# Kernel optimization log

Measured on AMD Instinct MI355X. Metric: run time of the kernel, lower is better.

Reference implementation:

```python
import jax, jax.numpy as jnp
import numpy as np

MAX_LEVEL = 3
FULL_LEN = 2 ** MAX_LEVEL  # wavelet_full_len for db1, mode='zero'


def _make_patterns():
    # Per-feature input to the DWT is [v, 0, ..., 0] (scalar zero-padded to 2**j).
    # Haar/db1 'zero' DWT of that signal is v times a fixed sparse pattern:
    # cA (len 1) = v*2^(-j/2); cD_k first element = v*2^(-k/2), rest zeros.
    pats = []
    for j in range(1, MAX_LEVEL + 1):
        vec = [2.0 ** (-j / 2.0)]                      # cA, length 1
        for k in range(1, j + 1):                      # cD_1 .. cD_j
            seg = np.zeros(2 ** (j - k))
            seg[0] = 2.0 ** (-k / 2.0)
            vec.extend(seg.tolist())
        full = np.zeros(FULL_LEN, dtype=np.float32)
        arr = np.asarray(vec, dtype=np.float32)
        full[: arr.shape[0]] = arr                     # F.pad to wavelet_full_len
        pats.append(full)
    return jnp.asarray(np.stack(pats))                 # (MAX_LEVEL, FULL_LEN)

_P = _make_patterns()


def _gumbel_hard(logits, gumb):
    # F.gumbel_softmax(logits, tau=1.0, hard=True), one sample per feature row.
    y = jax.nn.softmax(logits[None, :] + gumb, axis=-1)          # (feat, L)
    hard = jax.nn.one_hot(jnp.argmax(y, axis=-1), y.shape[-1], dtype=y.dtype)
    return jax.lax.stop_gradient(hard - y) + y                   # straight-through


def _wavelet_layer(x, logits, gumb, Wnl, bnl, Wwo, bwo):
    # Collapses the per-feature/per-level torch double loop:
    # xi_wave(level j) = v * (Wnl[f] . P[j]) + bnl[f]
    a = Wnl @ _P.T                       # (feat, levels)
    w = _gumbel_hard(logits, gumb)       # (feat, levels), one-hot rows
    coeff = jnp.sum(w * a, axis=-1)      # (feat,)
    agg = x * coeff + bnl                # (B, N, feat)
    return agg @ Wwo + bwo               # linear_out


def _mix(h, res_proj):
    diff = jnp.mean((h - res_proj) ** 2)
    th = jax.nn.sigmoid(diff)
    return th * h + (1.0 - th) * res_proj


def reference(x, adj, Wres, bres,
              Wg0, bg0, Wrg0, brg0, logits0, gumb0, Wnl0, bnl0, Wwo0, bwo0, Wrw0, brw0,
              Wg1, bg1, Wrg1, brg1, logits1, gumb1, Wnl1, bnl1, Wwo1, bwo1, Wrw1, brw1):
    res = x @ Wres + bres                                        # (B,N,Dout)
    # ---- layer 0 ----
    xg = jnp.einsum('ij,bjf->bif', adj, x) @ Wg0 + bg0           # 64->256: no residual add
    xg = _mix(xg, res @ Wrg0 + brg0)
    xw = _wavelet_layer(xg, logits0, gumb0, Wnl0, bnl0, Wwo0, bwo0) + xg  # 256==256: add
    xw = _mix(xw, res @ Wrw0 + brw0)
    # ---- layer 1 ----
    xg1 = jnp.einsum('ij,bjf->bif', adj, xw) @ Wg1 + bg1 + xw    # 256==256: add
    xg1 = _mix(xg1, res @ Wrg1 + brg1)
    xw1 = _wavelet_layer(xg1, logits1, gumb1, Wnl1, bnl1, Wwo1, bwo1)     # 256->64: no add
    xw1 = _mix(xw1, res @ Wrw1 + brw1)
    return xw1


def setup_inputs() -> dict:
    key = jax.random.key(0)
    ks = jax.random.split(key, 32)
    B, N, D_in, H, D_out = 128, 512, 64, 256, 64
    s = 0.05
    inp = {
        'x': jax.random.normal(ks[0], (B, N, D_in), jnp.float32),
        'adj': jax.random.uniform(ks[1], (N, N), jnp.float32) / N,
        'Wres': jax.random.normal(ks[2], (D_in, D_out), jnp.float32) * s,
        'bres': jax.random.normal(ks[3], (D_out,), jnp.float32) * s,
        'Wg0': jax.random.normal(ks[4], (D_in, H), jnp.float32) * s,
        'bg0': jax.random.normal(ks[5], (H,), jnp.float32) * s,
        'Wrg0': jax.random.normal(ks[6], (D_out, H), jnp.float32) * s,
        'brg0': jax.random.normal(ks[7], (H,), jnp.float32) * s,
        'logits0': jax.random.normal(ks[8], (3,), jnp.float32),
        'gumb0': jax.random.gumbel(ks[9], (H, 3), jnp.float32),
        'Wnl0': jax.random.normal(ks[10], (H, FULL_LEN), jnp.float32) * s,
        'bnl0': jax.random.normal(ks[11], (H,), jnp.float32) * s,
        'Wwo0': jax.random.normal(ks[12], (H, H), jnp.float32) * s,
        'bwo0': jax.random.normal(ks[13], (H,), jnp.float32) * s,
        'Wrw0': jax.random.normal(ks[14], (D_out, H), jnp.float32) * s,
        'brw0': jax.random.normal(ks[15], (H,), jnp.float32) * s,
        'Wg1': jax.random.normal(ks[16], (H, H), jnp.float32) * s,
        'bg1': jax.random.normal(ks[17], (H,), jnp.float32) * s,
        'Wrg1': jax.random.normal(ks[18], (D_out, H), jnp.float32) * s,
        'brg1': jax.random.normal(ks[19], (H,), jnp.float32) * s,
        'logits1': jax.random.normal(ks[20], (3,), jnp.float32),
        'gumb1': jax.random.gumbel(ks[21], (H, 3), jnp.float32),
        'Wnl1': jax.random.normal(ks[22], (H, FULL_LEN), jnp.float32) * s,
        'bnl1': jax.random.normal(ks[23], (H,), jnp.float32) * s,
        'Wwo1': jax.random.normal(ks[24], (H, D_out), jnp.float32) * s,
        'bwo1': jax.random.normal(ks[25], (D_out,), jnp.float32) * s,
        'Wrw1': jax.random.normal(ks[26], (D_out, D_out), jnp.float32) * s,
        'brw1': jax.random.normal(ks[27], (D_out,), jnp.float32) * s,
    }
    return inp
```

## Files before the change

### kernel.cpp

```cpp
#include <hip/hip_runtime.h>
#include <hip/hip_bf16.h>
#include <math.h>

#define BB   128
#define NN   512
#define DIN  64
#define HH   256
#define DOUT 64
#define BNR  (BB * NN)

typedef float  f32x4  __attribute__((ext_vector_type(4)));
typedef __bf16 bf16x8 __attribute__((ext_vector_type(8)));

#define GLP(p)  ((const __attribute__((address_space(1))) void*)(p))
#define LDSP(p) ((__attribute__((address_space(3))) void*)(p))

__constant__ float PAT[3][8] = {
    {0.70710678f, 0.70710678f, 0.f, 0.f, 0.f, 0.f, 0.f, 0.f},
    {0.5f,        0.70710678f, 0.f, 0.5f, 0.f, 0.f, 0.f, 0.f},
    {0.35355339f, 0.70710678f, 0.f, 0.f, 0.f, 0.5f, 0.f, 0.35355339f}
};

__device__ __forceinline__ unsigned short f2bfu(float x) {
    __hip_bfloat16 b = __float2bfloat16(x);
    unsigned short u;
    __builtin_memcpy(&u, &b, 2);
    return u;
}
__device__ __forceinline__ float bf2f(unsigned short u) {
    unsigned int v = ((unsigned int)u) << 16;
    float f;
    __builtin_memcpy(&f, &v, 4);
    return f;
}

__device__ __forceinline__ float block_th(const float* __restrict__ partial, int np,
                                          float inv_n, float* red, int tid)
{
    float s = 0.f;
    for (int i = tid; i < np; i += 256) s += partial[i];
    red[tid] = s;
    __syncthreads();
    for (int o = 128; o > 0; o >>= 1) {
        if (tid < o) red[tid] += red[tid + o];
        __syncthreads();
    }
    float th = 1.f / (1.f + expf(-red[0] * inv_n));
    __syncthreads();
    return th;
}

template<int BM, int BN, int FM, int FN>
__device__ __forceinline__ void write_tile(char* lds, f32x4 (&a)[FM][FN],
                                           __hip_bfloat16* __restrict__ C,
                                           long base, int N, int tid)
{
    const int wave = tid >> 6;
    const int lane = tid & 63;
    const int wm = wave >> 1, wn = wave & 1;
    const int lc = lane & 15;
    const int lr4 = (lane >> 4) << 2;
    __syncthreads();
    #pragma unroll
    for (int j = 0; j < FN; ++j) {
        int colb = (wn * (FN * 16) + j * 16 + lc) * 2;
        #pragma unroll
        for (int i = 0; i < FM; ++i) {
            int row0 = wm * (FM * 16) + i * 16 + lr4;
            #pragma unroll
            for (int r = 0; r < 4; ++r) {
                int row = row0 + r;
                *reinterpret_cast<unsigned short*>(
                    lds + row * (BN * 2) + (colb ^ (((row >> 2) & 3) << 5))) =
                    f2bfu(a[i][j][r]);
            }
        }
    }
    __syncthreads();
    const int TPR = BN / 8;
    const int RPP = 256 / TPR;
    #pragma unroll
    for (int p = 0; p < BM / RPP; ++p) {
        int row = p * RPP + tid / TPR;
        int cb = (tid % TPR) * 16;
        int pb = cb ^ (((row >> 2) & 3) << 5);
        uint4 v = *reinterpret_cast<const uint4*>(lds + row * (BN * 2) + pb);
        *reinterpret_cast<uint4*>(reinterpret_cast<char*>(C + base + (long)row * N) + cb) = v;
    }
}

template<int BM, int BN>
__device__ __forceinline__ void stage_tiles(const __hip_bfloat16* __restrict__ Ab,
                                            const __hip_bfloat16* __restrict__ Bb,
                                            char* AsB, char* BsB,
                                            int m0, int n0, int k0, int KA, int KB,
                                            int wave, int lane)
{
    const int NCH = (BM + BN) / 32;
    const int lr = lane >> 3;
    const int ls = lane & 7;
    #pragma unroll
    for (int cc = 0; cc < NCH; ++cc) {
        int c = wave * NCH + cc;
        const __hip_bfloat16* src;
        char* ldsb;
        if (c < BM / 8) {
            int r = c * 8 + lr;
            ldsb = AsB + c * 1024;
            src = Ab + ((long)(m0 + r) * KA + k0 + ((ls ^ (r & 7)) << 3));
        } else {
            int c2 = c - BM / 8;
            int r = c2 * 8 + lr;
            ldsb = BsB + c2 * 1024;
            src = Bb + ((long)(n0 + r) * KB + k0 + ((ls ^ (r & 7)) << 3));
        }
        __builtin_amdgcn_global_load_lds(GLP(src), LDSP(ldsb), 16, 0, 0);
    }
}

template<int BM, int BN, int FM, int FN>
__device__ __forceinline__ void mfma_tiles(char* AsB, char* BsB,
                                           f32x4 (&acc)[FM][FN], int wave, int lane)
{
    const int wm = wave >> 1, wn = wave & 1;
    #pragma unroll
    for (int ksl = 0; ksl < 2; ++ksl) {
        bf16x8 af[FM], bfr[FN];
        #pragma unroll
        for (int i = 0; i < FM; ++i) {
            int row = wm * (FM * 16) + i * 16 + (lane & 15);
            int off = (ksl * 64 + ((lane >> 4) << 4)) ^ ((row & 7) << 4);
            af[i] = *reinterpret_cast<const bf16x8*>(AsB + row * 128 + off);
        }
        #pragma unroll
        for (int j = 0; j < FN; ++j) {
            int row = wn * (FN * 16) + j * 16 + (lane & 15);
            int off = (ksl * 64 + ((lane >> 4) << 4)) ^ ((row & 7) << 4);
            bfr[j] = *reinterpret_cast<const bf16x8*>(BsB + row * 128 + off);
        }
        #pragma unroll
        for (int i = 0; i < FM; ++i)
            #pragma unroll
            for (int j = 0; j < FN; ++j)
                acc[i][j] = __builtin_amdgcn_mfma_f32_16x16x32_bf16(
                    af[i], bfr[j], acc[i][j], 0, 0, 0);
    }
}

__global__ __launch_bounds__(256) void cvt_k(const float* __restrict__ in,
                                             unsigned short* __restrict__ out, long n4)
{
    long gid = (long)blockIdx.x * 256 + threadIdx.x;
    long stride = (long)gridDim.x * 256;
    for (long i = gid; i < n4; i += stride) {
        float4 v = reinterpret_cast<const float4*>(in)[i];
        ushort4 u;
        u.x = f2bfu(v.x); u.y = f2bfu(v.y); u.z = f2bfu(v.z); u.w = f2bfu(v.w);
        reinterpret_cast<ushort4*>(out)[i] = u;
    }
}

__global__ __launch_bounds__(256) void cvtx_k(const float* __restrict__ in,
                                              unsigned short* __restrict__ rm,
                                              unsigned short* __restrict__ tr)
{
    __shared__ float t[64][65];
    const long base = (long)blockIdx.z * NN * DIN;
    const int r0 = blockIdx.y * 64;
    const int tr4 = threadIdx.x >> 6;
    const int tc  = threadIdx.x & 63;
    #pragma unroll
    for (int i = 0; i < 16; ++i) {
        int r = i * 4 + tr4;
        float v = in[base + (long)(r0 + r) * DIN + tc];
        t[r][tc] = v;
        rm[base + (long)(r0 + r) * DIN + tc] = f2bfu(v);
    }
    __syncthreads();
    #pragma unroll
    for (int i = 0; i < 16; ++i) {
        int d = i * 4 + tr4;
        tr[base + (long)d * NN + r0 + tc] = f2bfu(t[tc][d]);
    }
}

__device__ __forceinline__ void tcvt_body(const float* __restrict__ in,
                                          unsigned short* __restrict__ out,
                                          const float* __restrict__ cs, float us,
                                          int R, int C, int r0, int c0)
{
    __shared__ float t[64][65];
    int tr = threadIdx.x >> 6;
    int tc = threadIdx.x & 63;
    #pragma unroll
    for (int i = 0; i < 16; ++i) {
        int r = i * 4 + tr;
        t[r][tc] = in[(long)(r0 + r) * C + c0 + tc];
    }
    __syncthreads();
    float sc = (cs ? cs[r0 + tc] : 1.0f) * us;
    #pragma unroll
    for (int i = 0; i < 16; ++i) {
        int r = i * 4 + tr;
        out[(long)(c0 + r) * R + r0 + tc] = f2bfu(t[tc][r] * sc);
    }
}

struct WTArgs {
    const float* src[8];
    unsigned short* dst[8];
    const float* cs[8];
    float sgn[8];
    int R[8], C[8];
};
__global__ __launch_bounds__(256) void tcvt_w_k(WTArgs a)
{
    int wgt = blockIdx.y;
    int R = a.R[wgt], C = a.C[wgt];
    int tilesX = C >> 6;
    int tiles = (R >> 6) * tilesX;
    int t = blockIdx.x;
    if (t >= tiles) return;
    tcvt_body(a.src[wgt], a.dst[wgt], a.cs[wgt], a.sgn[wgt], R, C,
              (t / tilesX) * 64, (t % tilesX) * 64);
}

__global__ void coeff_k(const float* __restrict__ logits, const float* __restrict__ gumb,
                        const float* __restrict__ Wnl, float* __restrict__ coeff)
{
    int f = threadIdx.x;
    float l0 = logits[0] + gumb[f * 3 + 0];
    float l1 = logits[1] + gumb[f * 3 + 1];
    float l2 = logits[2] + gumb[f * 3 + 2];
    int bl = 0;
    float bv = l0;
    if (l1 > bv) { bv = l1; bl = 1; }
    if (l2 > bv) { bv = l2; bl = 2; }
    float s = 0.f;
    #pragma unroll
    for (int t = 0; t < 8; ++t) s += Wnl[f * 8 + t] * PAT[bl][t];
    coeff[f] = s;
}

struct FVArgs {
    const float* W[5];
    const float* c[5];
    const float* v[5];
    const float* base[5];
    float* out[5];
    int K[5], N[5];
};
__global__ __launch_bounds__(256) void foldvec_k(FVArgs a)
{
    int cs = blockIdx.y;
    int n = blockIdx.x;
    if (n >= a.N[cs]) return;
    int k = threadIdx.x;
    float s = 0.f;
    if (k < a.K[cs]) {
        float cc = a.c[cs] ? a.c[cs][k] : 1.0f;
        s = a.v[cs][k] * cc * a.W[cs][(long)k * a.N[cs] + n];
    }
    __shared__ float sm[256];
    sm[threadIdx.x] = s;
    __syncthreads();
    for (int o = 128; o > 0; o >>= 1) {
        if (threadIdx.x < o) sm[threadIdx.x] += sm[threadIdx.x + o];
        __syncthreads();
    }
    if (threadIdx.x == 0)
        a.out[cs][n] = (a.base[cs] ? a.base[cs][n] : 0.f) + sm[0];
}

struct WFArgs {
    const float* Wsrc[3];
    const float* Wbig[3];
    const float* c[3];
    int incl[3], N[3];
    unsigned short* dst[3];
};
__global__ __launch_bounds__(256) void wfold_k(WFArgs a)
{
    int cs = blockIdx.y;
    int m = blockIdx.x;
    __shared__ float ws[256];
    ws[threadIdx.x] = a.Wsrc[cs][m * 256 + threadIdx.x] * a.c[cs][threadIdx.x];
    __syncthreads();
    int n = threadIdx.x;
    int N = a.N[cs];
    if (n >= N) return;
    float s = a.incl[cs] ? a.Wsrc[cs][m * 256 + n] : 0.f;
    const float* Wb = a.Wbig[cs];
    #pragma unroll 8
    for (int k = 0; k < 256; ++k)
        s += ws[k] * Wb[(long)k * N + n];
    a.dst[cs][n * 64 + m] = f2bfu(s);
}

__global__ __launch_bounds__(256) void sc0_k(
    const float* __restrict__ partial, int np, float inv_n,
    unsigned short* __restrict__ Wa,
    unsigned short* __restrict__ Wb,
    const float* __restrict__ bg0p, const float* __restrict__ brg0p,
    const float* __restrict__ crow0, float* __restrict__ cv0)
{
    __shared__ float red[256];
    float th = block_th(partial, np, inv_n, red, threadIdx.x);
    float om = 1.f - th;
    int g = blockIdx.x * 256 + threadIdx.x;
    Wa[g] = f2bfu(th * bf2f(Wa[g]));
    Wb[g] = f2bfu(om * bf2f(Wb[g]));
    if (g < 256) cv0[g] = th * bg0p[g] + om * brg0p[g] + crow0[g];
}

__global__ __launch_bounds__(256) void sc1_k(
    const float* __restrict__ partial, int np, float inv_n,
    const unsigned short* __restrict__ Wrw0T, unsigned short* __restrict__ Wrw0sT,
    unsigned short* __restrict__ Wg0pT, unsigned short* __restrict__ Wrg0pT,
    const float* __restrict__ bg1, const float* __restrict__ brw0,
    const float* __restrict__ cv0, float* __restrict__ bv1g)
{
    __shared__ float red[256];
    float th = block_th(partial, np, inv_n, red, threadIdx.x);
    float om = 1.f - th;
    int g = blockIdx.x * 256 + threadIdx.x;
    Wrw0sT[g] = f2bfu(om * bf2f(Wrw0T[g]));
    Wg0pT[g]  = f2bfu(th * bf2f(Wg0pT[g]));
    Wrg0pT[g] = f2bfu(th * bf2f(Wrg0pT[g]));
    if (g < 256) bv1g[g] = bg1[g] + om * brw0[g] + th * cv0[g];
}

__global__ __launch_bounds__(256) void sc2_k(
    const float* __restrict__ partial, int np, float inv_n,
    unsigned short* __restrict__ Wc1T,
    unsigned short* __restrict__ Wrgc1T,
    const float* __restrict__ brgc1, const float* __restrict__ crow1,
    float* __restrict__ cv2)
{
    __shared__ float red[256];
    float th = block_th(partial, np, inv_n, red, threadIdx.x);
    float om = 1.f - th;
    int g = blockIdx.x * 256 + threadIdx.x;
    Wc1T[g] = f2bfu(th * bf2f(Wc1T[g]));
    if (g < 4096) Wrgc1T[g] = f2bfu(om * bf2f(Wrgc1T[g]));
    if (g < 64) cv2[g] = om * brgc1[g] + crow1[g];
}

template<int BM, int BN, int FM, int FN>
__global__ __launch_bounds__(256) void gemm_bt_k(
    const __hip_bfloat16* __restrict__ A, const __hip_bfloat16* __restrict__ Bt,
    const float* __restrict__ bias, __hip_bfloat16* __restrict__ Cb,
    int M, int N, int K)
{
    __shared__ __attribute__((aligned(128))) char lds[(BM + BN) * 128];
    char* AsB = lds;
    char* BsB = lds + BM * 128;

    const int m0 = blockIdx.y * BM;
    const int n0 = blockIdx.x * BN;
    const int tid  = threadIdx.x;
    const int wave = tid >> 6;
    const int lane = tid & 63;
    const int wn = wave & 1;

    f32x4 acc[FM][FN];
    #pragma unroll
    for (int i = 0; i < FM; ++i)
        #pragma unroll
        for (int j = 0; j < FN; ++j)
            acc[i][j] = (f32x4){0.f, 0.f, 0.f, 0.f};

    for (int k0 = 0; k0 < K; k0 += 64) {
        stage_tiles<BM, BN>(A, Bt, AsB, BsB, m0, n0, k0, K, K, wave, lane);
        __syncthreads();
        mfma_tiles<BM, BN, FM, FN>(AsB, BsB, acc, wave, lane);
        __syncthreads();
    }

    const int lc = lane & 15;
    #pragma unroll
    for (int j = 0; j < FN; ++j) {
        int col = n0 + wn * (FN * 16) + j * 16 + lc;
        float bv = bias ? bias[col] : 0.0f;
        #pragma unroll
        for (int i = 0; i < FM; ++i)
            #pragma unroll
            for (int r = 0; r < 4; ++r)
                acc[i][j][r] += bv;
    }
    write_tile<BM, BN, FM, FN>(lds, acc, Cb, (long)m0 * N + n0, N, tid);
}

template<int BM, int BN, int FM, int FN, int GX, int NB>
__global__ __launch_bounds__(256) void gemm_bt_swz_k(
    const __hip_bfloat16* __restrict__ A, const __hip_bfloat16* __restrict__ Bt,
    __hip_bfloat16* __restrict__ Cb,
    int M, int N, int K, long sA, long sB, long sC)
{
    __shared__ __attribute__((aligned(128))) char lds[(BM + BN) * 128];
    char* AsB = lds;
    char* BsB = lds + BM * 128;

    const int d   = blockIdx.x;
    const int xcd = d & 7;
    const int q   = d >> 3;
    const int t   = q % NB;
    const int bz  = xcd + ((q / NB) << 3);
    const int n0  = (t % GX) * BN;
    const int m0  = (t / GX) * BM;

    const __hip_bfloat16* Ab = A + (long)bz * sA;
    const __hip_bfloat16* Bb = Bt + (long)bz * sB;

    const int tid  = threadIdx.x;
    const int wave = tid >> 6;
    const int lane = tid & 63;
    const int wn = wave & 1;

    f32x4 acc[FM][FN];
    #pragma unroll
    for (int i = 0; i < FM; ++i)
        #pragma unroll
        for (int j = 0; j < FN; ++j)
            acc[i][j] = (f32x4){0.f, 0.f, 0.f, 0.f};

    for (int k0 = 0; k0 < K; k0 += 64) {
        stage_tiles<BM, BN>(Ab, Bb, AsB, BsB, m0, n0, k0, K, K, wave, lane);
        __syncthreads();
        mfma_tiles<BM, BN, FM, FN>(AsB, BsB, acc, wave, lane);
        __syncthreads();
    }

    write_tile<BM, BN, FM, FN>(lds, acc, Cb, (long)bz * sC + (long)m0 * N + n0, N, tid);
}

template<int BM, int BN, int FM, int FN>
__global__ __launch_bounds__(256) void dual1_k(
    const __hip_bfloat16* __restrict__ A0, const __hip_bfloat16* __restrict__ B0, int K0,
    const __hip_bfloat16* __restrict__ A1, const __hip_bfloat16* __restrict__ B1, int K1,
    const float* __restrict__ b1, const float* __restrict__ b2,
    float* __restrict__ partial, int M, int N)
{
    __shared__ __attribute__((aligned(128))) char lds[(BM + BN) * 128];
    char* AsB = lds;
    char* BsB = lds + BM * 128;

    const int d   = blockIdx.x;
    const int q   = d >> 3;
    const int nx  = q & 1;
    const int my  = (d & 7) + ((q >> 1) << 3);
    const int m0  = my * BM;
    const int n0  = nx * BN;

    const int tid  = threadIdx.x;
    const int wave = tid >> 6;
    const int lane = tid & 63;
    const int wn = wave & 1;

    f32x4 acc[FM][FN];
    #pragma unroll
    for (int i = 0; i < FM; ++i)
        #pragma unroll
        for (int j = 0; j < FN; ++j)
            acc[i][j] = (f32x4){0.f, 0.f, 0.f, 0.f};

    #pragma unroll
    for (int ph = 0; ph < 2; ++ph) {
        const __hip_bfloat16* Ab = ph ? A1 : A0;
        const __hip_bfloat16* Bb = ph ? B1 : B0;
        const int K = ph ? K1 : K0;
        for (int k0 = 0; k0 < K; k0 += 64) {
            stage_tiles<BM, BN>(Ab, Bb, AsB, BsB, m0, n0, k0, K, K, wave, lane);
            __syncthreads();
            mfma_tiles<BM, BN, FM, FN>(AsB, BsB, acc, wave, lane);
            __syncthreads();
        }
    }

    const int lc = lane & 15;
    float dsum = 0.f;
    #pragma unroll
    for (int j = 0; j < FN; ++j) {
        int col = n0 + wn * (FN * 16) + j * 16 + lc;
        float bd = b1[col] - b2[col];
        #pragma unroll
        for (int i = 0; i < FM; ++i)
            #pragma unroll
            for (int r = 0; r < 4; ++r) {
                float dd = acc[i][j][r] + bd;
                dsum += dd * dd;
            }
    }

    float* red = (float*)lds;
    red[tid] = dsum;
    __syncthreads();
    for (int o = 128; o > 0; o >>= 1) {
        if (tid < o) red[tid] += red[tid + o];
        __syncthreads();
    }
    if (tid == 0) partial[my * 2 + nx] = red[0];
}

template<int BM, int BN, int FM, int FN, bool SWZ>
__global__ __launch_bounds__(256) void wave2_k(
    const __hip_bfloat16* __restrict__ A0, const __hip_bfloat16* __restrict__ B0, int K0,
    const __hip_bfloat16* __restrict__ A1, const __hip_bfloat16* __restrict__ B1, int K1,
    const __hip_bfloat16* __restrict__ A2, const __hip_bfloat16* __restrict__ B2, int K2,
    const float* __restrict__ cv, const float* __restrict__ b2v,
    __hip_bfloat16* __restrict__ C1, __hip_bfloat16* __restrict__ C2,
    float* __restrict__ partial_out, int M, int N)
{
    __shared__ __attribute__((aligned(128))) char lds[(BM + BN) * 128];
    char* AsB = lds;
    char* BsB = lds + BM * 128;

    int m0, n0, pidx;
    if constexpr (SWZ) {
        const int d = blockIdx.x;
        const int q = d >> 3;
        const int nx = q & 1;
        const int my = (d & 7) + ((q >> 1) << 3);
        m0 = my * BM; n0 = nx * BN; pidx = my * 2 + nx;
    } else {
        m0 = blockIdx.y * BM; n0 = blockIdx.x * BN;
        pidx = blockIdx.y * gridDim.x + blockIdx.x;
    }

    const int tid  = threadIdx.x;
    const int wave = tid >> 6;
    const int lane = tid & 63;
    const int wn = wave & 1;

    f32x4 acc0[FM][FN], acc1[FM][FN];
    #pragma unroll
    for (int i = 0; i < FM; ++i)
        #pragma unroll
        for (int j = 0; j < FN; ++j) {
            acc0[i][j] = (f32x4){0.f, 0.f, 0.f, 0.f};
            acc1[i][j] = (f32x4){0.f, 0.f, 0.f, 0.f};
        }

    #pragma unroll
    for (int ph = 0; ph < 3; ++ph) {
        const __hip_bfloat16* Ab = (ph == 0) ? A0 : (ph == 1 ? A1 : A2);
        const __hip_bfloat16* Bb = (ph == 0) ? B0 : (ph == 1 ? B1 : B2);
        const int K = (ph == 0) ? K0 : (ph == 1 ? K1 : K2);
        for (int k0 = 0; k0 < K; k0 += 64) {
            stage_tiles<BM, BN>(Ab, Bb, AsB, BsB, m0, n0, k0, K, K, wave, lane);
            __syncthreads();
            if (ph < 2) mfma_tiles<BM, BN, FM, FN>(AsB, BsB, acc0, wave, lane);
            else        mfma_tiles<BM, BN, FM, FN>(AsB, BsB, acc1, wave, lane);
            __syncthreads();
        }
    }

    const int lc = lane & 15;
    float dsum = 0.f;
    #pragma unroll
    for (int j = 0; j < FN; ++j) {
        int col = n0 + wn * (FN * 16) + j * 16 + lc;
        float c1 = cv[col];
        float c2 = b2v[col];
        #pragma unroll
        for (int i = 0; i < FM; ++i)
            #pragma unroll
            for (int r = 0; r < 4; ++r) {
                float v1 = acc0[i][j][r] + c1;
                float v2 = acc1[i][j][r] + c2;
                acc0[i][j][r] = v1;
                acc1[i][j][r] = v2;
                float dd = v1 - v2;
                dsum += dd * dd;
            }
    }

    float* red = (float*)lds;
    red[tid] = dsum;
    __syncthreads();
    for (int o = 128; o > 0; o >>= 1) {
        if (tid < o) red[tid] += red[tid + o];
        __syncthreads();
    }
    if (tid == 0) partial_out[pidx] = red[0];

    write_tile<BM, BN, FM, FN>(lds, acc0, C1, (long)m0 * N + n0, N, tid);
    write_tile<BM, BN, FM, FN>(lds, acc1, C2, (long)m0 * N + n0, N, tid);
}

template<int BM, int BN, int FM, int FN>
__global__ __launch_bounds__(256) void gmix3_k(
    const __hip_bfloat16* __restrict__ A0, const __hip_bfloat16* __restrict__ B0, int K0,
    const __hip_bfloat16* __restrict__ A1, const __hip_bfloat16* __restrict__ B1, int K1,
    const __hip_bfloat16* __restrict__ A2, const __hip_bfloat16* __restrict__ B2, int K2,
    const __hip_bfloat16* __restrict__ A3, const __hip_bfloat16* __restrict__ B3, int K3,
    const __hip_bfloat16* __restrict__ A4, const __hip_bfloat16* __restrict__ B4, int K4,
    const float* __restrict__ bv1, const float* __restrict__ b2v,
    __hip_bfloat16* __restrict__ C1, float* __restrict__ partial_out, int M, int N)
{
    __shared__ __attribute__((aligned(128))) char lds[(BM + BN) * 128];
    char* AsB = lds;
    char* BsB = lds + BM * 128;

    const int d  = blockIdx.x;
    const int q  = d >> 3;
    const int nx = q & 1;
    const int my = (d & 7) + ((q >> 1) << 3);
    const int m0 = my * BM;
    const int n0 = nx * BN;

    const int tid  = threadIdx.x;
    const int wave = tid >> 6;
    const int lane = tid & 63;
    const int wn = wave & 1;

    f32x4 acc0[FM][FN], acc1[FM][FN];
    #pragma unroll
    for (int i = 0; i < FM; ++i)
        #pragma unroll
        for (int j = 0; j < FN; ++j) {
            acc0[i][j] = (f32x4){0.f, 0.f, 0.f, 0.f};
            acc1[i][j] = (f32x4){0.f, 0.f, 0.f, 0.f};
        }

    const __hip_bfloat16* As[5] = {A0, A1, A2, A3, A4};
    const __hip_bfloat16* Bs[5] = {B0, B1, B2, B3, B4};
    const int Ks[5] = {K0, K1, K2, K3, K4};

    #pragma unroll
    for (int ph = 0; ph < 5; ++ph) {
        const __hip_bfloat16* Ab = As[ph];
        const __hip_bfloat16* Bb = Bs[ph];
        const int K = Ks[ph];
        for (int k0 = 0; k0 < K; k0 += 64) {
            stage_tiles<BM, BN>(Ab, Bb, AsB, BsB, m0, n0, k0, K, K, wave, lane);
            __syncthreads();
            if (ph < 4) mfma_tiles<BM, BN, FM, FN>(AsB, BsB, acc0, wave, lane);
            else        mfma_tiles<BM, BN, FM, FN>(AsB, BsB, acc1, wave, lane);
            __syncthreads();
        }
    }

    const int lc = lane & 15;
    float dsum = 0.f;
    #pragma unroll
    for (int j = 0; j < FN; ++j) {
        int col = n0 + wn * (FN * 16) + j * 16 + lc;
        float c1 = bv1[col];
        float c2 = b2v[col];
        #pragma unroll
        for (int i = 0; i < FM; ++i)
            #pragma unroll
            for (int r = 0; r < 4; ++r) {
                float v1 = acc0[i][j][r] + c1;
                float v2 = acc1[i][j][r] + c2;
                acc0[i][j][r] = v1;
                float dd = v1 - v2;
                dsum += dd * dd;
            }
    }

    float* red = (float*)lds;
    red[tid] = dsum;
    __syncthreads();
    for (int o = 128; o > 0; o >>= 1) {
        if (tid < o) red[tid] += red[tid + o];
        __syncthreads();
    }
    if (tid == 0) partial_out[my * 2 + nx] = red[0];

    write_tile<BM, BN, FM, FN>(lds, acc0, C1, (long)m0 * N + n0, N, tid);
}

__global__ __launch_bounds__(256) void mixT_k(
    const unsigned short* __restrict__ h, const unsigned short* __restrict__ r,
    const float* __restrict__ partial_in, int np_in, float inv_in,
    unsigned short* __restrict__ xwT)
{
    __shared__ float t[64][65];
    const float th = block_th(partial_in, np_in, inv_in, &t[0][0], (int)threadIdx.x);
    const float om = 1.f - th;
    const long base = (long)blockIdx.z * NN * HH;
    const int r0 = blockIdx.y * 64;
    const int c0 = blockIdx.x * 64;
    const int tr  = threadIdx.x >> 4;
    const int tc4 = (threadIdx.x & 15) * 4;
    #pragma unroll
    for (int i = 0; i < 4; ++i) {
        int rr = i * 16 + tr;
        long idx = base + (long)(r0 + rr) * HH + c0 + tc4;
        ushort4 hv = *reinterpret_cast<const ushort4*>(h + idx);
        ushort4 rv = *reinterpret_cast<const ushort4*>(r + idx);
        t[rr][tc4 + 0] = th * bf2f(hv.x) + om * bf2f(rv.x);
        t[rr][tc4 + 1] = th * bf2f(hv.y) + om * bf2f(rv.y);
        t[rr][tc4 + 2] = th * bf2f(hv.z) + om * bf2f(rv.z);
        t[rr][tc4 + 3] = th * bf2f(hv.w) + om * bf2f(rv.w);
    }
    __syncthreads();
    #pragma unroll
    for (int i = 0; i < 4; ++i) {
        int cc = i * 16 + tr;
        ushort4 v;
        v.x = f2bfu(t[tc4 + 0][cc]);
        v.y = f2bfu(t[tc4 + 1][cc]);
        v.z = f2bfu(t[tc4 + 2][cc]);
        v.w = f2bfu(t[tc4 + 3][cc]);
        *reinterpret_cast<ushort4*>(xwT + base + (long)(c0 + cc) * NN + r0 + tc4) = v;
    }
}

__global__ __launch_bounds__(256) void mixfinal_k(
    const unsigned short* __restrict__ h, const unsigned short* __restrict__ r,
    const float* __restrict__ partial_in, int np_in, float inv_in,
    float* __restrict__ out, long n4)
{
    __shared__ float sm[256];
    const float th = block_th(partial_in, np_in, inv_in, sm, (int)threadIdx.x);
    const float om = 1.f - th;
    long gid = (long)blockIdx.x * 256 + threadIdx.x;
    long stride = (long)gridDim.x * 256;
    for (long i = gid; i < n4; i += stride) {
        ushort4 hv = reinterpret_cast<const ushort4*>(h)[i];
        ushort4 rv = reinterpret_cast<const ushort4*>(r)[i];
        float4 o;
        o.x = th * bf2f(hv.x) + om * bf2f(rv.x);
        o.y = th * bf2f(hv.y) + om * bf2f(rv.y);
        o.z = th * bf2f(hv.z) + om * bf2f(rv.z);
        o.w = th * bf2f(hv.w) + om * bf2f(rv.w);
        reinterpret_cast<float4*>(out)[i] = o;
    }
}

extern "C" void kernel_launch(void* const* d_in, const int* in_sizes, int n_in,
                              void* d_out, int out_size, void* d_ws, size_t ws_size,
                              hipStream_t stream)
{
    const float* x       = (const float*)d_in[0];
    const float* adj     = (const float*)d_in[1];
    const float* Wres    = (const float*)d_in[2];
    const float* bres    = (const float*)d_in[3];
    const float* Wg0     = (const float*)d_in[4];
    const float* bg0     = (const float*)d_in[5];
    const float* Wrg0    = (const float*)d_in[6];
    const float* brg0    = (const float*)d_in[7];
    const float* logits0 = (const float*)d_in[8];
    const float* gumb0   = (const float*)d_in[9];
    const float* Wnl0    = (const float*)d_in[10];
    const float* bnl0    = (const float*)d_in[11];
    const float* Wwo0    = (const float*)d_in[12];
    const float* bwo0    = (const float*)d_in[13];
    const float* Wrw0    = (const float*)d_in[14];
    const float* brw0    = (const float*)d_in[15];
    const float* Wg1     = (const float*)d_in[16];
    const float* bg1     = (const float*)d_in[17];
    const float* Wrg1    = (const float*)d_in[18];
    const float* brg1    = (const float*)d_in[19];
    const float* logits1 = (const float*)d_in[20];
    const float* gumb1   = (const float*)d_in[21];
    const float* Wnl1    = (const float*)d_in[22];
    const float* bnl1    = (const float*)d_in[23];
    const float* Wwo1    = (const float*)d_in[24];
    const float* bwo1    = (const float*)d_in[25];
    const float* Wrw1    = (const float*)d_in[26];
    const float* brw1    = (const float*)d_in[27];

    float* out = (float*)d_out;

    char* w = (char*)d_ws;
    auto alloc = [&](long bytes) { char* p = w; w += (bytes + 255) & ~255L; return p; };
    const long SLOT = (long)BNR * HH * 2;
    char* pool = alloc(5 * SLOT);
    __hip_bfloat16* Rbf  = (__hip_bfloat16*)alloc((long)BNR * DOUT * 2);
    __hip_bfloat16* adjb = (__hip_bfloat16*)alloc((long)NN * NN * 2);
    __hip_bfloat16* WT   = (__hip_bfloat16*)alloc(208896L * 2);
    float* partial0 = (float*)alloc(2048 * 4);
    float* partial1 = (float*)alloc(2048 * 4);
    float* partial2 = (float*)alloc(2048 * 4);
    float* partial3 = (float*)alloc(2048 * 4);
    float* c0      = (float*)alloc(256 * 4);
    float* c1      = (float*)alloc(256 * 4);
    float* bg0p    = (float*)alloc(256 * 4);
    float* brg0p   = (float*)alloc(256 * 4);
    float* crow0   = (float*)alloc(256 * 4);
    float* brgc1   = (float*)alloc(64 * 4);
    float* crow1   = (float*)alloc(64 * 4);
    float* cv0     = (float*)alloc(256 * 4);
    float* bv1g    = (float*)alloc(256 * 4);
    float* cv2     = (float*)alloc(64 * 4);

    auto S = [&](int i) { return pool + (long)i * SLOT; };
    __hip_bfloat16* xwr = (__hip_bfloat16*)S(0);
    __hip_bfloat16* rw0 = (__hip_bfloat16*)S(1);
    __hip_bfloat16* orw = (__hip_bfloat16*)S(1);
    __hip_bfloat16* rw1 = (__hip_bfloat16*)(S(1) + (long)BNR * DOUT * 2);
    __hip_bfloat16* xwT = (__hip_bfloat16*)S(2);
    __hip_bfloat16* xg1 = (__hip_bfloat16*)S(2);
    __hip_bfloat16* T1  = (__hip_bfloat16*)S(3);
    __hip_bfloat16* xbf = (__hip_bfloat16*)S(4);
    __hip_bfloat16* xT  = (__hip_bfloat16*)(S(4) + (long)BNR * DIN * 2);
    __hip_bfloat16* T0  = (__hip_bfloat16*)(S(4) + 2L * BNR * DIN * 2);

    __hip_bfloat16* WresT  = WT;
    __hip_bfloat16* Wg0T   = WT + 4096;
    __hip_bfloat16* Wrg0T  = WT + 20480;
    __hip_bfloat16* Wrw0T  = WT + 36864;
    __hip_bfloat16* Wg1T   = WT + 53248;
    __hip_bfloat16* Wrg1T  = WT + 118784;
    __hip_bfloat16* Wc1T   = WT + 135168;
    __hip_bfloat16* Wrw1T  = WT + 151552;
    __hip_bfloat16* Wg0pT  = WT + 155648;
    __hip_bfloat16* Wrg0pT = WT + 172032;
    __hip_bfloat16* Wrgc1T = WT + 188416;
    __hip_bfloat16* Wrw0sT = WT + 192512;

    const dim3 blk(256);
    const float invH = 1.0f / ((float)BNR * HH);
    const float invD = 1.0f / ((float)BNR * DOUT);

    hipLaunchKernelGGL(coeff_k, dim3(1), dim3(256), 0, stream, logits0, gumb0, Wnl0, c0);
    hipLaunchKernelGGL(coeff_k, dim3(1), dim3(256), 0, stream, logits1, gumb1, Wnl1, c1);
    hipLaunchKernelGGL(cvt_k, dim3(256), blk, 0, stream, adj, (unsigned short*)adjb, (long)NN * NN / 4);
    hipLaunchKernelGGL(cvtx_k, dim3(1, 8, BB), blk, 0, stream, x,
                       (unsigned short*)xbf, (unsigned short*)xT);

    WTArgs wa;
    wa.src[0] = Wres; wa.dst[0] = (unsigned short*)WresT; wa.cs[0] = nullptr; wa.sgn[0] = 1.f;  wa.R[0] = 64;  wa.C[0] = 64;
    wa.src[1] = Wg0;  wa.dst[1] = (unsigned short*)Wg0T;  wa.cs[1] = nullptr; wa.sgn[1] = 1.f;  wa.R[1] = 64;  wa.C[1] = 256;
    wa.src[2] = Wrg0; wa.dst[2] = (unsigned short*)Wrg0T; wa.cs[2] = nullptr; wa.sgn[2] = -1.f; wa.R[2] = 64;  wa.C[2] = 256;
    wa.src[3] = Wrw0; wa.dst[3] = (unsigned short*)Wrw0T; wa.cs[3] = nullptr; wa.sgn[3] = 1.f;  wa.R[3] = 64;  wa.C[3] = 256;
    wa.src[4] = Wg1;  wa.dst[4] = (unsigned short*)Wg1T;  wa.cs[4] = nullptr; wa.sgn[4] = 1.f;  wa.R[4] = 256; wa.C[4] = 256;
    wa.src[5] = Wrg1; wa.dst[5] = (unsigned short*)Wrg1T; wa.cs[5] = nullptr; wa.sgn[5] = 1.f;  wa.R[5] = 64;  wa.C[5] = 256;
    wa.src[6] = Wwo1; wa.dst[6] = (unsigned short*)Wc1T;  wa.cs[6] = c1;      wa.sgn[6] = 1.f;  wa.R[6] = 256; wa.C[6] = 64;
    wa.src[7] = Wrw1; wa.dst[7] = (unsigned short*)Wrw1T; wa.cs[7] = nullptr; wa.sgn[7] = 1.f;  wa.R[7] = 64;  wa.C[7] = 64;
    hipLaunchKernelGGL(tcvt_w_k, dim3(16, 8), blk, 0, stream, wa);

    WFArgs wf;
    wf.Wsrc[0] = Wg0;  wf.Wbig[0] = Wwo0; wf.c[0] = c0; wf.incl[0] = 1; wf.N[0] = 256;
    wf.dst[0] = (unsigned short*)Wg0pT;
    wf.Wsrc[1] = Wrg0; wf.Wbig[1] = Wwo0; wf.c[1] = c0; wf.incl[1] = 1; wf.N[1] = 256;
    wf.dst[1] = (unsigned short*)Wrg0pT;
    wf.Wsrc[2] = Wrg1; wf.Wbig[2] = Wwo1; wf.c[2] = c1; wf.incl[2] = 0; wf.N[2] = 64;
    wf.dst[2] = (unsigned short*)Wrgc1T;
    hipLaunchKernelGGL(wfold_k, dim3(64, 3), blk, 0, stream, wf);

    FVArgs fv;
    fv.W[0] = Wwo0; fv.c[0] = c0;      fv.v[0] = bg0;  fv.base[0] = bg0;  fv.out[0] = bg0p;  fv.K[0] = 256; fv.N[0] = 256;
    fv.W[1] = Wwo0; fv.c[1] = c0;      fv.v[1] = brg0; fv.base[1] = brg0; fv.out[1] = brg0p; fv.K[1] = 256; fv.N[1] = 256;
    fv.W[2] = Wwo0; fv.c[2] = nullptr; fv.v[2] = bnl0; fv.base[2] = bwo0; fv.out[2] = crow0; fv.K[2] = 256; fv.N[2] = 256;
    fv.W[3] = Wwo1; fv.c[3] = c1;      fv.v[3] = brg1; fv.base[3] = nullptr; fv.out[3] = brgc1; fv.K[3] = 256; fv.N[3] = 64;
    fv.W[4] = Wwo1; fv.c[4] = nullptr; fv.v[4] = bnl1; fv.base[4] = bwo1; fv.out[4] = crow1; fv.K[4] = 256; fv.N[4] = 64;
    hipLaunchKernelGGL(foldvec_k, dim3(256, 5), blk, 0, stream, fv);

    hipLaunchKernelGGL((gemm_bt_k<128, 64, 4, 2>), dim3(1, BNR / 128, 1), blk, 0, stream,
                       xbf, WresT, bres, Rbf, BNR, DOUT, DIN);

    hipLaunchKernelGGL((gemm_bt_swz_k<128, 64, 4, 2, 1, 4>), dim3(BB * 4), blk, 0, stream,
                       adjb, xT, T0, NN, DIN, NN, 0, (long)DIN * NN, (long)NN * DIN);

    hipLaunchKernelGGL((dual1_k<64, 128, 2, 4>), dim3(2 * BNR / 64), blk, 0, stream,
                       T0, Wg0T, DIN, Rbf, Wrg0T, DOUT, bg0, brg0, partial0, BNR, HH);

    hipLaunchKernelGGL(sc0_k, dim3(64), blk, 0, stream, partial0, 2048, invH,
                       (unsigned short*)Wg0pT, (unsigned short*)Wrg0pT,
                       bg0p, brg0p, crow0, cv0);

    hipLaunchKernelGGL((wave2_k<64, 128, 2, 4, true>), dim3(2 * BNR / 64), blk, 0, stream,
                       T0, Wg0pT, DIN, Rbf, Wrg0pT, DOUT, Rbf, Wrw0T, DOUT,
                       cv0, brw0, xwr, rw0, partial1, BNR, HH);

    hipLaunchKernelGGL(sc1_k, dim3(64), blk, 0, stream, partial1, 2048, invH,
                       (const unsigned short*)Wrw0T, (unsigned short*)Wrw0sT,
                       (unsigned short*)Wg0pT, (unsigned short*)Wrg0pT,
                       bg1, brw0, cv0, bv1g);

    hipLaunchKernelGGL(mixT_k, dim3(4, 8, BB), blk, 0, stream,
                       (const unsigned short*)xwr, (const unsigned short*)rw0,
                       partial1, 2048, invH, (unsigned short*)xwT);

    hipLaunchKernelGGL((gemm_bt_swz_k<128, 128, 4, 4, 2, 8>), dim3(BB * 8), blk, 0, stream,
                       adjb, xwT, T1, NN, HH, NN, 0, (long)HH * NN, (long)NN * HH);

    hipLaunchKernelGGL((gmix3_k<64, 128, 2, 4>), dim3(2 * BNR / 64), blk, 0, stream,
                       T1, Wg1T, HH,
                       Rbf, Wrw0sT, DOUT,
                       T0, Wg0pT, DIN,
                       Rbf, Wrg0pT, DOUT,
                       Rbf, Wrg1T, DOUT,
                       bv1g, brg1, xg1, partial2, BNR, HH);

    hipLaunchKernelGGL(sc2_k, dim3(64), blk, 0, stream, partial2, 2048, invH,
                       (unsigned short*)Wc1T, (unsigned short*)Wrgc1T,
                       brgc1, crow1, cv2);

    hipLaunchKernelGGL((wave2_k<64, 64, 2, 2, false>), dim3(1, BNR / 64), blk, 0, stream,
                       xg1, Wc1T, HH, Rbf, Wrgc1T, DOUT, Rbf, Wrw1T, DIN,
                       cv2, brw1, orw, rw1, partial3, BNR, DOUT);

    hipLaunchKernelGGL(mixfinal_k, dim3(2048), blk, 0, stream,
                       (const unsigned short*)orw, (const unsigned short*)rw1,
                       partial3, 1024, invD, out, (long)BNR * DOUT / 4);
}
```

Before: 197.5 us.

## Fold layer-1 mix through adjacency algebraically, eliminating the mixT transpose pass

The first-layer mix (th*xw + (1-th)*rw0) is no longer materialized before the adjacency GEMM. wave2T now writes only the xw branch, already transposed, straight into the B operand of the adjacency GEMM. The residual branch is carried separately: adj@(Rbf@Wrw0@Wg1) is computed as (adj@Rbf) times a prefolded weight, and the bias is handled through adjacency row sums. This drops the mixT_k kernel and the rw0 store, and merges the two coeff launches. In exchange it adds an extra adjacency GEMM over the residual, a transposed residual write, a sixth MFMA phase in the mix kernel, and more bf16 rounding from prefolded weights.

```diff
diff --git a/kernel.cpp b/kernel.cpp
--- a/kernel.cpp
+++ b/kernel.cpp
@@ -86,6 +86,46 @@
         int pb = cb ^ (((row >> 2) & 3) << 5);
         uint4 v = *reinterpret_cast<const uint4*>(lds + row * (BN * 2) + pb);
         *reinterpret_cast<uint4*>(reinterpret_cast<char*>(C + base + (long)row * N) + cb) = v;
+    }
+}
+
+template<int BM, int BN, int FM, int FN>
+__device__ __forceinline__ void write_tileT(char* lds, f32x4 (&a)[FM][FN],
+                                            __hip_bfloat16* __restrict__ CT,
+                                            long baseT, int ldT, int tid)
+{
+    const int wave = tid >> 6;
+    const int lane = tid & 63;
+    const int wm = wave >> 1, wn = wave & 1;
+    const int lc = lane & 15;
+    const int lr4 = (lane >> 4) << 2;
+    __syncthreads();
+    #pragma unroll
+    for (int j = 0; j < FN; ++j) {
+        int c = wn * (FN * 16) + j * 16 + lc;
+        int cbase = c * (BM * 2);
+        int swz = ((c >> 2) & 3) << 5;
+        #pragma unroll
+        for (int i = 0; i < FM; ++i) {
+            int m0 = wm * (FM * 16) + i * 16 + lr4;
+            #pragma unroll
+            for (int r = 0; r < 4; ++r) {
+                int m = m0 + r;
+                *reinterpret_cast<unsigned short*>(lds + cbase + ((m * 2) ^ swz)) =
+                    f2bfu(a[i][j][r]);
+            }
+        }
+    }
+    __syncthreads();
+    const int TPR = BM / 8;
+    const int RPP = 256 / TPR;
+    #pragma unroll
+    for (int p = 0; p < BN / RPP; ++p) {
+        int c = p * RPP + tid / TPR;
+        int tb = (tid % TPR) * 16;
+        int pb = tb ^ (((c >> 2) & 3) << 5);
+        uint4 v = *reinterpret_cast<const uint4*>(lds + c * (BM * 2) + pb);
+        *reinterpret_cast<uint4*>(reinterpret_cast<char*>(CT + baseT + (long)c * ldT) + tb) = v;
     }
 }
 
@@ -147,17 +187,22 @@
     }
 }
 
-__global__ __launch_bounds__(256) void cvt_k(const float* __restrict__ in,
-                                             unsigned short* __restrict__ out, long n4)
-{
-    long gid = (long)blockIdx.x * 256 + threadIdx.x;
-    long stride = (long)gridDim.x * 256;
-    for (long i = gid; i < n4; i += stride) {
-        float4 v = reinterpret_cast<const float4*>(in)[i];
-        ushort4 u;
-        u.x = f2bfu(v.x); u.y = f2bfu(v.y); u.z = f2bfu(v.z); u.w = f2bfu(v.w);
-        reinterpret_cast<ushort4*>(out)[i] = u;
-    }
+__global__ __launch_bounds__(256) void cvta_k(const float* __restrict__ adj,
+                                              unsigned int* __restrict__ adjb,
+                                              float* __restrict__ ars)
+{
+    int n = blockIdx.x;
+    int t = threadIdx.x;
+    float2 v = reinterpret_cast<const float2*>(adj)[n * 256 + t];
+    adjb[n * 256 + t] = (unsigned int)f2bfu(v.x) | ((unsigned int)f2bfu(v.y) << 16);
+    __shared__ float sm[256];
+    sm[t] = v.x + v.y;
+    __syncthreads();
+    for (int o = 128; o > 0; o >>= 1) {
+        if (t < o) sm[t] += sm[t + o];
+        __syncthreads();
+    }
+    if (t == 0) ars[n] = sm[0];
 }
 
 __global__ __launch_bounds__(256) void cvtx_k(const float* __restrict__ in,
@@ -225,30 +270,36 @@
               (t / tilesX) * 64, (t % tilesX) * 64);
 }
 
-__global__ void coeff_k(const float* __restrict__ logits, const float* __restrict__ gumb,
-                        const float* __restrict__ Wnl, float* __restrict__ coeff)
-{
+__global__ void coeff2_k(const float* __restrict__ logits0, const float* __restrict__ gumb0,
+                         const float* __restrict__ Wnl0, float* __restrict__ c0,
+                         const float* __restrict__ logits1, const float* __restrict__ gumb1,
+                         const float* __restrict__ Wnl1, float* __restrict__ c1)
+{
+    const float* lg = blockIdx.x ? logits1 : logits0;
+    const float* gb = blockIdx.x ? gumb1 : gumb0;
+    const float* Wn = blockIdx.x ? Wnl1 : Wnl0;
+    float* cc = blockIdx.x ? c1 : c0;
     int f = threadIdx.x;
-    float l0 = logits[0] + gumb[f * 3 + 0];
-    float l1 = logits[1] + gumb[f * 3 + 1];
-    float l2 = logits[2] + gumb[f * 3 + 2];
+    float l0 = lg[0] + gb[f * 3 + 0];
+    float l1 = lg[1] + gb[f * 3 + 1];
+    float l2 = lg[2] + gb[f * 3 + 2];
     int bl = 0;
     float bv = l0;
     if (l1 > bv) { bv = l1; bl = 1; }
     if (l2 > bv) { bv = l2; bl = 2; }
     float s = 0.f;
     #pragma unroll
-    for (int t = 0; t < 8; ++t) s += Wnl[f * 8 + t] * PAT[bl][t];
-    coeff[f] = s;
+    for (int t = 0; t < 8; ++t) s += Wn[f * 8 + t] * PAT[bl][t];
+    cc[f] = s;
 }
 
 struct FVArgs {
-    const float* W[5];
-    const float* c[5];
-    const float* v[5];
-    const float* base[5];
-    float* out[5];
-    int K[5], N[5];
+    const float* W[6];
+    const float* c[6];
+    const float* v[6];
+    const float* base[6];
+    float* out[6];
+    int K[6], N[6];
 };
 __global__ __launch_bounds__(256) void foldvec_k(FVArgs a)
 {
@@ -273,18 +324,19 @@
 }
 
 struct WFArgs {
-    const float* Wsrc[3];
-    const float* Wbig[3];
-    const float* c[3];
-    int incl[3], N[3];
-    unsigned short* dst[3];
+    const float* Wsrc[4];
+    const float* Wbig[4];
+    const float* c[4];
+    int incl[4], N[4];
+    unsigned short* dst[4];
 };
 __global__ __launch_bounds__(256) void wfold_k(WFArgs a)
 {
     int cs = blockIdx.y;
     int m = blockIdx.x;
     __shared__ float ws[256];
-    ws[threadIdx.x] = a.Wsrc[cs][m * 256 + threadIdx.x] * a.c[cs][threadIdx.x];
+    const float* c = a.c[cs];
+    ws[threadIdx.x] = a.Wsrc[cs][m * 256 + threadIdx.x] * (c ? c[threadIdx.x] : 1.0f);
     __syncthreads();
     int n = threadIdx.x;
     int N = a.N[cs];
@@ -315,19 +367,29 @@
 
 __global__ __launch_bounds__(256) void sc1_k(
     const float* __restrict__ partial, int np, float inv_n,
+    unsigned short* __restrict__ Wg1T,
     const unsigned short* __restrict__ Wrw0T, unsigned short* __restrict__ Wrw0sT,
     unsigned short* __restrict__ Wg0pT, unsigned short* __restrict__ Wrg0pT,
+    unsigned short* __restrict__ WrwWg1T,
     const float* __restrict__ bg1, const float* __restrict__ brw0,
-    const float* __restrict__ cv0, float* __restrict__ bv1g)
+    const float* __restrict__ cv0, const float* __restrict__ bw1v,
+    float* __restrict__ bv1g, float* __restrict__ bw1s)
 {
     __shared__ float red[256];
     float th = block_th(partial, np, inv_n, red, threadIdx.x);
     float om = 1.f - th;
     int g = blockIdx.x * 256 + threadIdx.x;
-    Wrw0sT[g] = f2bfu(om * bf2f(Wrw0T[g]));
-    Wg0pT[g]  = f2bfu(th * bf2f(Wg0pT[g]));
-    Wrg0pT[g] = f2bfu(th * bf2f(Wrg0pT[g]));
-    if (g < 256) bv1g[g] = bg1[g] + om * brw0[g] + th * cv0[g];
+    Wg1T[g] = f2bfu(th * bf2f(Wg1T[g]));
+    if (g < 16384) {
+        Wrw0sT[g]  = f2bfu(om * bf2f(Wrw0T[g]));
+        Wg0pT[g]   = f2bfu(th * bf2f(Wg0pT[g]));
+        Wrg0pT[g]  = f2bfu(th * bf2f(Wrg0pT[g]));
+        WrwWg1T[g] = f2bfu(om * bf2f(WrwWg1T[g]));
+    }
+    if (g < 256) {
+        bv1g[g] = bg1[g] + om * brw0[g] + th * cv0[g];
+        bw1s[g] = om * bw1v[g];
+    }
 }
 
 __global__ __launch_bounds__(256) void sc2_k(
@@ -347,9 +409,10 @@
 }
 
 template<int BM, int BN, int FM, int FN>
-__global__ __launch_bounds__(256) void gemm_bt_k(
+__global__ __launch_bounds__(256) void gemm_res_k(
     const __hip_bfloat16* __restrict__ A, const __hip_bfloat16* __restrict__ Bt,
-    const float* __restrict__ bias, __hip_bfloat16* __restrict__ Cb,
+    const float* __restrict__ bias,
+    __hip_bfloat16* __restrict__ Cb, __hip_bfloat16* __restrict__ CbT,
     int M, int N, int K)
 {
     __shared__ __attribute__((aligned(128))) char lds[(BM + BN) * 128];
@@ -357,7 +420,7 @@
     char* BsB = lds + BM * 128;
 
     const int m0 = blockIdx.y * BM;
-    const int n0 = blockIdx.x * BN;
+    const int n0 = 0;
     const int tid  = threadIdx.x;
     const int wave = tid >> 6;
     const int lane = tid & 63;
@@ -380,8 +443,7 @@
     const int lc = lane & 15;
     #pragma unroll
     for (int j = 0; j < FN; ++j) {
-        int col = n0 + wn * (FN * 16) + j * 16 + lc;
-        float bv = bias ? bias[col] : 0.0f;
+        float bv = bias[n0 + wn * (FN * 16) + j * 16 + lc];
         #pragma unroll
         for (int i = 0; i < FM; ++i)
             #pragma unroll
@@ -389,6 +451,8 @@
                 acc[i][j][r] += bv;
     }
     write_tile<BM, BN, FM, FN>(lds, acc, Cb, (long)m0 * N + n0, N, tid);
+    long baseT = (long)(m0 / NN) * ((long)N * NN) + (m0 % NN);
+    write_tileT<BM, BN, FM, FN>(lds, acc, CbT, baseT, NN, tid);
 }
 
 template<int BM, int BN, int FM, int FN, int GX, int NB>
@@ -415,7 +479,6 @@
     const int tid  = threadIdx.x;
     const int wave = tid >> 6;
     const int lane = tid & 63;
-    const int wn = wave & 1;
 
     f32x4 acc[FM][FN];
     #pragma unroll
@@ -502,30 +565,24 @@
     if (tid == 0) partial[my * 2 + nx] = red[0];
 }
 
-template<int BM, int BN, int FM, int FN, bool SWZ>
-__global__ __launch_bounds__(256) void wave2_k(
+template<int BM, int BN, int FM, int FN>
+__global__ __launch_bounds__(256) void wave2T_k(
     const __hip_bfloat16* __restrict__ A0, const __hip_bfloat16* __restrict__ B0, int K0,
     const __hip_bfloat16* __restrict__ A1, const __hip_bfloat16* __restrict__ B1, int K1,
     const __hip_bfloat16* __restrict__ A2, const __hip_bfloat16* __restrict__ B2, int K2,
     const float* __restrict__ cv, const float* __restrict__ b2v,
-    __hip_bfloat16* __restrict__ C1, __hip_bfloat16* __restrict__ C2,
-    float* __restrict__ partial_out, int M, int N)
+    __hip_bfloat16* __restrict__ C1T, float* __restrict__ partial_out, int M, int N)
 {
     __shared__ __attribute__((aligned(128))) char lds[(BM + BN) * 128];
     char* AsB = lds;
     char* BsB = lds + BM * 128;
 
-    int m0, n0, pidx;
-    if constexpr (SWZ) {
-        const int d = blockIdx.x;
-        const int q = d >> 3;
-        const int nx = q & 1;
-        const int my = (d & 7) + ((q >> 1) << 3);
-        m0 = my * BM; n0 = nx * BN; pidx = my * 2 + nx;
-    } else {
-        m0 = blockIdx.y * BM; n0 = blockIdx.x * BN;
-        pidx = blockIdx.y * gridDim.x + blockIdx.x;
-    }
+    const int d   = blockIdx.x;
+    const int q   = d >> 3;
+    const int nx  = q & 1;
+    const int my  = (d & 7) + ((q >> 1) << 3);
+    const int m0  = my * BM;
+    const int n0  = nx * BN;
 
     const int tid  = threadIdx.x;
     const int wave = tid >> 6;
@@ -569,7 +626,6 @@
                 float v1 = acc0[i][j][r] + c1;
                 float v2 = acc1[i][j][r] + c2;
                 acc0[i][j][r] = v1;
-                acc1[i][j][r] = v2;
                 float dd = v1 - v2;
                 dsum += dd * dd;
             }
@@ -582,20 +638,22 @@
         if (tid < o) red[tid] += red[tid + o];
         __syncthreads();
     }
-    if (tid == 0) partial_out[pidx] = red[0];
-
-    write_tile<BM, BN, FM, FN>(lds, acc0, C1, (long)m0 * N + n0, N, tid);
-    write_tile<BM, BN, FM, FN>(lds, acc1, C2, (long)m0 * N + n0, N, tid);
+    if (tid == 0) partial_out[my * 2 + nx] = red[0];
+
+    long baseT = (long)(m0 / NN) * ((long)N * NN) + (long)n0 * NN + (m0 % NN);
+    write_tileT<BM, BN, FM, FN>(lds, acc0, C1T, baseT, NN, tid);
 }
 
 template<int BM, int BN, int FM, int FN>
-__global__ __launch_bounds__(256) void gmix3_k(
+__global__ __launch_bounds__(256) void gmix4_k(
     const __hip_bfloat16* __restrict__ A0, const __hip_bfloat16* __restrict__ B0, int K0,
     const __hip_bfloat16* __restrict__ A1, const __hip_bfloat16* __restrict__ B1, int K1,
     const __hip_bfloat16* __restrict__ A2, const __hip_bfloat16* __restrict__ B2, int K2,
     const __hip_bfloat16* __restrict__ A3, const __hip_bfloat16* __restrict__ B3, int K3,
     const __hip_bfloat16* __restrict__ A4, const __hip_bfloat16* __restrict__ B4, int K4,
+    const __hip_bfloat16* __restrict__ A5, const __hip_bfloat16* __restrict__ B5, int K5,
     const float* __restrict__ bv1, const float* __restrict__ b2v,
+    const float* __restrict__ ars, const float* __restrict__ bw1s,
     __hip_bfloat16* __restrict__ C1, float* __restrict__ partial_out, int M, int N)
 {
     __shared__ __attribute__((aligned(128))) char lds[(BM + BN) * 128];
@@ -612,7 +670,7 @@
     const int tid  = threadIdx.x;
     const int wave = tid >> 6;
     const int lane = tid & 63;
-    const int wn = wave & 1;
+    const int wm = wave >> 1, wn = wave & 1;
 
     f32x4 acc0[FM][FN], acc1[FM][FN];
     #pragma unroll
@@ -623,30 +681,112 @@
             acc1[i][j] = (f32x4){0.f, 0.f, 0.f, 0.f};
         }
 
-    const __hip_bfloat16* As[5] = {A0, A1, A2, A3, A4};
-    const __hip_bfloat16* Bs[5] = {B0, B1, B2, B3, B4};
-    const int Ks[5] = {K0, K1, K2, K3, K4};
-
-    #pragma unroll
-    for (int ph = 0; ph < 5; ++ph) {
+    const __hip_bfloat16* As[6] = {A0, A1, A2, A3, A4, A5};
+    const __hip_bfloat16* Bs[6] = {B0, B1, B2, B3, B4, B5};
+    const int Ks[6] = {K0, K1, K2, K3, K4, K5};
+
+    #pragma unroll
+    for (int ph = 0; ph < 6; ++ph) {
         const __hip_bfloat16* Ab = As[ph];
         const __hip_bfloat16* Bb = Bs[ph];
         const int K = Ks[ph];
         for (int k0 = 0; k0 < K; k0 += 64) {
             stage_tiles<BM, BN>(Ab, Bb, AsB, BsB, m0, n0, k0, K, K, wave, lane);
             __syncthreads();
-            if (ph < 4) mfma_tiles<BM, BN, FM, FN>(AsB, BsB, acc0, wave, lane);
+            if (ph < 5) mfma_tiles<BM, BN, FM, FN>(AsB, BsB, acc0, wave, lane);
             else        mfma_tiles<BM, BN, FM, FN>(AsB, BsB, acc1, wave, lane);
             __syncthreads();
         }
     }
 
-    const int lc = lane & 15;
+    const int lc  = lane & 15;
+    const int lr4 = (lane >> 4) << 2;
+    const int node0 = m0 & (NN - 1);
     float dsum = 0.f;
     #pragma unroll
     for (int j = 0; j < FN; ++j) {
         int col = n0 + wn * (FN * 16) + j * 16 + lc;
         float c1 = bv1[col];
+        float c2 = b2v[col];
+        float bw = bw1s[col];
+        #pragma unroll
+        for (int i = 0; i < FM; ++i) {
+            int rowl = wm * (FM * 16) + i * 16 + lr4;
+            #pragma unroll
+            for (int r = 0; r < 4; ++r) {
+                float av = ars[node0 + rowl + r];
+                float v1 = acc0[i][j][r] + c1 + av * bw;
+                float v2 = acc1[i][j][r] + c2;
+                acc0[i][j][r] = v1;
+                float dd = v1 - v2;
+                dsum += dd * dd;
+            }
+        }
+    }
+
+    float* red = (float*)lds;
+    red[tid] = dsum;
+    __syncthreads();
+    for (int o = 128; o > 0; o >>= 1) {
+        if (tid < o) red[tid] += red[tid + o];
+        __syncthreads();
+    }
+    if (tid == 0) partial_out[my * 2 + nx] = red[0];
+
+    write_tile<BM, BN, FM, FN>(lds, acc0, C1, (long)m0 * N + n0, N, tid);
+}
+
+template<int BM, int BN, int FM, int FN>
+__global__ __launch_bounds__(256) void wave2_k(
+    const __hip_bfloat16* __restrict__ A0, const __hip_bfloat16* __restrict__ B0, int K0,
+    const __hip_bfloat16* __restrict__ A1, const __hip_bfloat16* __restrict__ B1, int K1,
+    const __hip_bfloat16* __restrict__ A2, const __hip_bfloat16* __restrict__ B2, int K2,
+    const float* __restrict__ cv, const float* __restrict__ b2v,
+    __hip_bfloat16* __restrict__ C1, __hip_bfloat16* __restrict__ C2,
+    float* __restrict__ partial_out, int M, int N)
+{
+    __shared__ __attribute__((aligned(128))) char lds[(BM + BN) * 128];
+    char* AsB = lds;
+    char* BsB = lds + BM * 128;
+
+    const int m0 = blockIdx.y * BM;
+    const int n0 = blockIdx.x * BN;
+    const int pidx = blockIdx.y * gridDim.x + blockIdx.x;
+
+    const int tid  = threadIdx.x;
+    const int wave = tid >> 6;
+    const int lane = tid & 63;
+    const int wn = wave & 1;
+
+    f32x4 acc0[FM][FN], acc1[FM][FN];
+    #pragma unroll
+    for (int i = 0; i < FM; ++i)
+        #pragma unroll
+        for (int j = 0; j < FN; ++j) {
+            acc0[i][j] = (f32x4){0.f, 0.f, 0.f, 0.f};
+            acc1[i][j] = (f32x4){0.f, 0.f, 0.f, 0.f};
+        }
+
+    #pragma unroll
+    for (int ph = 0; ph < 3; ++ph) {
+        const __hip_bfloat16* Ab = (ph == 0) ? A0 : (ph == 1 ? A1 : A2);
+        const __hip_bfloat16* Bb = (ph == 0) ? B0 : (ph == 1 ? B1 : B2);
+        const int K = (ph == 0) ? K0 : (ph == 1 ? K1 : K2);
+        for (int k0 = 0; k0 < K; k0 += 64) {
+            stage_tiles<BM, BN>(Ab, Bb, AsB, BsB, m0, n0, k0, K, K, wave, lane);
+            __syncthreads();
+            if (ph < 2) mfma_tiles<BM, BN, FM, FN>(AsB, BsB, acc0, wave, lane);
+            else        mfma_tiles<BM, BN, FM, FN>(AsB, BsB, acc1, wave, lane);
+            __syncthreads();
+        }
+    }
+
+    const int lc = lane & 15;
+    float dsum = 0.f;
+    #pragma unroll
+    for (int j = 0; j < FN; ++j) {
+        int col = n0 + wn * (FN * 16) + j * 16 + lc;
+        float c1 = cv[col];
         float c2 = b2v[col];
         #pragma unroll
         for (int i = 0; i < FM; ++i)
@@ -655,6 +795,7 @@
                 float v1 = acc0[i][j][r] + c1;
                 float v2 = acc1[i][j][r] + c2;
                 acc0[i][j][r] = v1;
+                acc1[i][j][r] = v2;
                 float dd = v1 - v2;
                 dsum += dd * dd;
             }
@@ -667,46 +808,10 @@
         if (tid < o) red[tid] += red[tid + o];
         __syncthreads();
     }
-    if (tid == 0) partial_out[my * 2 + nx] = red[0];
+    if (tid == 0) partial_out[pidx] = red[0];
 
     write_tile<BM, BN, FM, FN>(lds, acc0, C1, (long)m0 * N + n0, N, tid);
-}
-
-__global__ __launch_bounds__(256) void mixT_k(
-    const unsigned short* __restrict__ h, const unsigned short* __restrict__ r,
-    const float* __restrict__ partial_in, int np_in, float inv_in,
-    unsigned short* __restrict__ xwT)
-{
-    __shared__ float t[64][65];
-    const float th = block_th(partial_in, np_in, inv_in, &t[0][0], (int)threadIdx.x);
-    const float om = 1.f - th;
-    const long base = (long)blockIdx.z * NN * HH;
-    const int r0 = blockIdx.y * 64;
-    const int c0 = blockIdx.x * 64;
-    const int tr  = threadIdx.x >> 4;
-    const int tc4 = (threadIdx.x & 15) * 4;
-    #pragma unroll
-    for (int i = 0; i < 4; ++i) {
-        int rr = i * 16 + tr;
-        long idx = base + (long)(r0 + rr) * HH + c0 + tc4;
-        ushort4 hv = *reinterpret_cast<const ushort4*>(h + idx);
-        ushort4 rv = *reinterpret_cast<const ushort4*>(r + idx);
-        t[rr][tc4 + 0] = th * bf2f(hv.x) + om * bf2f(rv.x);
-        t[rr][tc4 + 1] = th * bf2f(hv.y) + om * bf2f(rv.y);
-        t[rr][tc4 + 2] = th * bf2f(hv.z) + om * bf2f(rv.z);
-        t[rr][tc4 + 3] = th * bf2f(hv.w) + om * bf2f(rv.w);
-    }
-    __syncthreads();
-    #pragma unroll
-    for (int i = 0; i < 4; ++i) {
-        int cc = i * 16 + tr;
-        ushort4 v;
-        v.x = f2bfu(t[tc4 + 0][cc]);
-        v.y = f2bfu(t[tc4 + 1][cc]);
-        v.z = f2bfu(t[tc4 + 2][cc]);
-        v.w = f2bfu(t[tc4 + 3][cc]);
-        *reinterpret_cast<ushort4*>(xwT + base + (long)(c0 + cc) * NN + r0 + tc4) = v;
-    }
+    write_tile<BM, BN, FM, FN>(lds, acc1, C2, (long)m0 * N + n0, N, tid);
 }
 
 __global__ __launch_bounds__(256) void mixfinal_k(
@@ -772,7 +877,7 @@
     char* pool = alloc(5 * SLOT);
     __hip_bfloat16* Rbf  = (__hip_bfloat16*)alloc((long)BNR * DOUT * 2);
     __hip_bfloat16* adjb = (__hip_bfloat16*)alloc((long)NN * NN * 2);
-    __hip_bfloat16* WT   = (__hip_bfloat16*)alloc(208896L * 2);
+    __hip_bfloat16* WT   = (__hip_bfloat16*)alloc(225280L * 2);
     float* partial0 = (float*)alloc(2048 * 4);
     float* partial1 = (float*)alloc(2048 * 4);
     float* partial2 = (float*)alloc(2048 * 4);
@@ -787,39 +892,43 @@
     float* cv0     = (float*)alloc(256 * 4);
     float* bv1g    = (float*)alloc(256 * 4);
     float* cv2     = (float*)alloc(64 * 4);
+    float* ars     = (float*)alloc(512 * 4);
+    float* bw1v    = (float*)alloc(256 * 4);
+    float* bw1s    = (float*)alloc(256 * 4);
 
     auto S = [&](int i) { return pool + (long)i * SLOT; };
-    __hip_bfloat16* xwr = (__hip_bfloat16*)S(0);
-    __hip_bfloat16* rw0 = (__hip_bfloat16*)S(1);
-    __hip_bfloat16* orw = (__hip_bfloat16*)S(1);
-    __hip_bfloat16* rw1 = (__hip_bfloat16*)(S(1) + (long)BNR * DOUT * 2);
-    __hip_bfloat16* xwT = (__hip_bfloat16*)S(2);
-    __hip_bfloat16* xg1 = (__hip_bfloat16*)S(2);
-    __hip_bfloat16* T1  = (__hip_bfloat16*)S(3);
-    __hip_bfloat16* xbf = (__hip_bfloat16*)S(4);
-    __hip_bfloat16* xT  = (__hip_bfloat16*)(S(4) + (long)BNR * DIN * 2);
-    __hip_bfloat16* T0  = (__hip_bfloat16*)(S(4) + 2L * BNR * DIN * 2);
-
-    __hip_bfloat16* WresT  = WT;
-    __hip_bfloat16* Wg0T   = WT + 4096;
-    __hip_bfloat16* Wrg0T  = WT + 20480;
-    __hip_bfloat16* Wrw0T  = WT + 36864;
-    __hip_bfloat16* Wg1T   = WT + 53248;
-    __hip_bfloat16* Wrg1T  = WT + 118784;
-    __hip_bfloat16* Wc1T   = WT + 135168;
-    __hip_bfloat16* Wrw1T  = WT + 151552;
-    __hip_bfloat16* Wg0pT  = WT + 155648;
-    __hip_bfloat16* Wrg0pT = WT + 172032;
-    __hip_bfloat16* Wrgc1T = WT + 188416;
-    __hip_bfloat16* Wrw0sT = WT + 192512;
+    __hip_bfloat16* xwrT = (__hip_bfloat16*)S(0);
+    __hip_bfloat16* orw  = (__hip_bfloat16*)S(1);
+    __hip_bfloat16* rw1  = (__hip_bfloat16*)(S(1) + (long)BNR * DOUT * 2);
+    __hip_bfloat16* Radj = (__hip_bfloat16*)(S(1) + 2L * BNR * DOUT * 2);
+    __hip_bfloat16* xg1  = (__hip_bfloat16*)S(2);
+    __hip_bfloat16* T1x  = (__hip_bfloat16*)S(3);
+    __hip_bfloat16* xbf  = (__hip_bfloat16*)S(4);
+    __hip_bfloat16* xT   = (__hip_bfloat16*)(S(4) + (long)BNR * DIN * 2);
+    __hip_bfloat16* T0   = (__hip_bfloat16*)(S(4) + 2L * BNR * DIN * 2);
+    __hip_bfloat16* RbfT = (__hip_bfloat16*)(S(4) + 3L * BNR * DIN * 2);
+
+    __hip_bfloat16* WresT   = WT;
+    __hip_bfloat16* Wg0T    = WT + 4096;
+    __hip_bfloat16* Wrg0T   = WT + 20480;
+    __hip_bfloat16* Wrw0T   = WT + 36864;
+    __hip_bfloat16* Wg1T    = WT + 53248;
+    __hip_bfloat16* Wrg1T   = WT + 118784;
+    __hip_bfloat16* Wc1T    = WT + 135168;
+    __hip_bfloat16* Wrw1T   = WT + 151552;
+    __hip_bfloat16* Wg0pT   = WT + 155648;
+    __hip_bfloat16* Wrg0pT  = WT + 172032;
+    __hip_bfloat16* Wrgc1T  = WT + 188416;
+    __hip_bfloat16* Wrw0sT  = WT + 192512;
+    __hip_bfloat16* WrwWg1T = WT + 208896;
 
     const dim3 blk(256);
     const float invH = 1.0f / ((float)BNR * HH);
     const float invD = 1.0f / ((float)BNR * DOUT);
 
-    hipLaunchKernelGGL(coeff_k, dim3(1), dim3(256), 0, stream, logits0, gumb0, Wnl0, c0);
-    hipLaunchKernelGGL(coeff_k, dim3(1), dim3(256), 0, stream, logits1, gumb1, Wnl1, c1);
-    hipLaunchKernelGGL(cvt_k, dim3(256), blk, 0, stream, adj, (unsigned short*)adjb, (long)NN * NN / 4);
+    hipLaunchKernelGGL(coeff2_k, dim3(2), dim3(256), 0, stream,
+                       logits0, gumb0, Wnl0, c0, logits1, gumb1, Wnl1, c1);
+    hipLaunchKernelGGL(cvta_k, dim3(NN), blk, 0, stream, adj, (unsigned int*)adjb, ars);
     hipLaunchKernelGGL(cvtx_k, dim3(1, 8, BB), blk, 0, stream, x,
                        (unsigned short*)xbf, (unsigned short*)xT);
 
@@ -835,27 +944,33 @@
     hipLaunchKernelGGL(tcvt_w_k, dim3(16, 8), blk, 0, stream, wa);
 
     WFArgs wf;
-    wf.Wsrc[0] = Wg0;  wf.Wbig[0] = Wwo0; wf.c[0] = c0; wf.incl[0] = 1; wf.N[0] = 256;
+    wf.Wsrc[0] = Wg0;  wf.Wbig[0] = Wwo0; wf.c[0] = c0;      wf.incl[0] = 1; wf.N[0] = 256;
     wf.dst[0] = (unsigned short*)Wg0pT;
-    wf.Wsrc[1] = Wrg0; wf.Wbig[1] = Wwo0; wf.c[1] = c0; wf.incl[1] = 1; wf.N[1] = 256;
+    wf.Wsrc[1] = Wrg0; wf.Wbig[1] = Wwo0; wf.c[1] = c0;      wf.incl[1] = 1; wf.N[1] = 256;
     wf.dst[1] = (unsigned short*)Wrg0pT;
-    wf.Wsrc[2] = Wrg1; wf.Wbig[2] = Wwo1; wf.c[2] = c1; wf.incl[2] = 0; wf.N[2] = 64;
+    wf.Wsrc[2] = Wrg1; wf.Wbig[2] = Wwo1; wf.c[2] = c1;      wf.incl[2] = 0; wf.N[2] = 64;
     wf.dst[2] = (unsigned short*)Wrgc1T;
-    hipLaunchKernelGGL(wfold_k, dim3(64, 3), blk, 0, stream, wf);
+    wf.Wsrc[3] = Wrw0; wf.Wbig[3] = Wg1;  wf.c[3] = nullptr; wf.incl[3] = 0; wf.N[3] = 256;
+    wf.dst[3] = (unsigned short*)WrwWg1T;
+    hipLaunchKernelGGL(wfold_k, dim3(64, 4), blk, 0, stream, wf);
 
     FVArgs fv;
-    fv.W[0] = Wwo0; fv.c[0] = c0;      fv.v[0] = bg0;  fv.base[0] = bg0;  fv.out[0] = bg0p;  fv.K[0] = 256; fv.N[0] = 256;
-    fv.W[1] = Wwo0; fv.c[1] = c0;      fv.v[1] = brg0; fv.base[1] = brg0; fv.out[1] = brg0p; fv.K[1] = 256; fv.N[1] = 256;
-    fv.W[2] = Wwo0; fv.c[2] = nullptr; fv.v[2] = bnl0; fv.base[2] = bwo0; fv.out[2] = crow0; fv.K[2] = 256; fv.N[2] = 256;
+    fv.W[0] = Wwo0; fv.c[0] = c0;      fv.v[0] = bg0;  fv.base[0] = bg0;     fv.out[0] = bg0p;  fv.K[0] = 256; fv.N[0] = 256;
+    fv.W[1] = Wwo0; fv.c[1] = c0;      fv.v[1] = brg0; fv.base[1] = brg0;    fv.out[1] = brg0p; fv.K[1] = 256; fv.N[1] = 256;
+    fv.W[2] = Wwo0; fv.c[2] = nullptr; fv.v[2] = bnl0; fv.base[2] = bwo0;    fv.out[2] = crow0; fv.K[2] = 256; fv.N[2] = 256;
     fv.W[3] = Wwo1; fv.c[3] = c1;      fv.v[3] = brg1; fv.base[3] = nullptr; fv.out[3] = brgc1; fv.K[3] = 256; fv.N[3] = 64;
-    fv.W[4] = Wwo1; fv.c[4] = nullptr; fv.v[4] = bnl1; fv.base[4] = bwo1; fv.out[4] = crow1; fv.K[4] = 256; fv.N[4] = 64;
-    hipLaunchKernelGGL(foldvec_k, dim3(256, 5), blk, 0, stream, fv);
-
-    hipLaunchKernelGGL((gemm_bt_k<128, 64, 4, 2>), dim3(1, BNR / 128, 1), blk, 0, stream,
-                       xbf, WresT, bres, Rbf, BNR, DOUT, DIN);
+    fv.W[4] = Wwo1; fv.c[4] = nullptr; fv.v[4] = bnl1; fv.base[4] = bwo1;    fv.out[4] = crow1; fv.K[4] = 256; fv.N[4] = 64;
+    fv.W[5] = Wg1;  fv.c[5] = nullptr; fv.v[5] = brw0; fv.base[5] = nullptr; fv.out[5] = bw1v;  fv.K[5] = 256; fv.N[5] = 256;
+    hipLaunchKernelGGL(foldvec_k, dim3(256, 6), blk, 0, stream, fv);
+
+    hipLaunchKernelGGL((gemm_res_k<128, 64, 4, 2>), dim3(1, BNR / 128, 1), blk, 0, stream,
+                       xbf, WresT, bres, Rbf, RbfT, BNR, DOUT, DIN);
 
     hipLaunchKernelGGL((gemm_bt_swz_k<128, 64, 4, 2, 1, 4>), dim3(BB * 4), blk, 0, stream,
                        adjb, xT, T0, NN, DIN, NN, 0, (long)DIN * NN, (long)NN * DIN);
+
+    hipLaunchKernelGGL((gemm_bt_swz_k<128, 64, 4, 2, 1, 4>), dim3(BB * 4), blk, 0, stream,
+                       adjb, RbfT, Radj, NN, DOUT, NN, 0, (long)DOUT * NN, (long)NN * DOUT);
 
     hipLaunchKernelGGL((dual1_k<64, 128, 2, 4>), dim3(2 * BNR / 64), blk, 0, stream,
                        T0, Wg0T, DIN, Rbf, Wrg0T, DOUT, bg0, brg0, partial0, BNR, HH);
@@ -864,35 +979,34 @@
                        (unsigned short*)Wg0pT, (unsigned short*)Wrg0pT,
                        bg0p, brg0p, crow0, cv0);
 
-    hipLaunchKernelGGL((wave2_k<64, 128, 2, 4, true>), dim3(2 * BNR / 64), blk, 0, stream,
+    hipLaunchKernelGGL((wave2T_k<64, 128, 2, 4>), dim3(2 * BNR / 64), blk, 0, stream,
                        T0, Wg0pT, DIN, Rbf, Wrg0pT, DOUT, Rbf, Wrw0T, DOUT,
-                       cv0, brw0, xwr, rw0, partial1, BNR, HH);
-
-    hipLaunchKernelGGL(sc1_k, dim3(64), blk, 0, stream, partial1, 2048, invH,
+                       cv0, brw0, xwrT, partial1, BNR, HH);
+
+    hipLaunchKernelGGL(sc1_k, dim3(256), blk, 0, stream, partial1, 2048, invH,
+                       (unsigned short*)Wg1T,
                        (const unsigned short*)Wrw0T, (unsigned short*)Wrw0sT,
                        (unsigned short*)Wg0pT, (unsigned short*)Wrg0pT,
-                       bg1, brw0, cv0, bv1g);
-
-    hipLaunchKernelGGL(mixT_k, dim3(4, 8, BB), blk, 0, stream,
-                       (const unsigned short*)xwr, (const unsigned short*)rw0,
-                       partial1, 2048, invH, (unsigned short*)xwT);
+                       (unsigned short*)WrwWg1T,
+                       bg1, brw0, cv0, bw1v, bv1g, bw1s);
 
     hipLaunchKernelGGL((gemm_bt_swz_k<128, 128, 4, 4, 2, 8>), dim3(BB * 8), blk, 0, stream,
-                       adjb, xwT, T1, NN, HH, NN, 0, (long)HH * NN, (long)NN * HH);
-
-    hipLaunchKernelGGL((gmix3_k<64, 128, 2, 4>), dim3(2 * BNR / 64), blk, 0, stream,
-                       T1, Wg1T, HH,
-                       Rbf, Wrw0sT, DOUT,
+                       adjb, xwrT, T1x, NN, HH, NN, 0, (long)HH * NN, (long)NN * HH);
+
+    hipLaunchKernelGGL((gmix4_k<64, 128, 2, 4>), dim3(2 * BNR / 64), blk, 0, stream,
+                       T1x, Wg1T, HH,
+                       Radj, WrwWg1T, DOUT,
                        T0, Wg0pT, DIN,
                        Rbf, Wrg0pT, DOUT,
+                       Rbf, Wrw0sT, DOUT,
                        Rbf, Wrg1T, DOUT,
-                       bv1g, brg1, xg1, partial2, BNR, HH);
+                       bv1g, brg1, ars, bw1s, xg1, partial2, BNR, HH);
 
     hipLaunchKernelGGL(sc2_k, dim3(64), blk, 0, stream, partial2, 2048, invH,
                        (unsigned short*)Wc1T, (unsigned short*)Wrgc1T,
                        brgc1, crow1, cv2);
 
-    hipLaunchKernelGGL((wave2_k<64, 64, 2, 2, false>), dim3(1, BNR / 64), blk, 0, stream,
+    hipLaunchKernelGGL((wave2_k<64, 64, 2, 2>), dim3(1, BNR / 64), blk, 0, stream,
                        xg1, Wc1T, HH, Rbf, Wrgc1T, DOUT, Rbf, Wrw1T, DIN,
                        cv2, brw1, orw, rw1, partial3, BNR, DOUT);
 
```

New measurement: 194.2 us. About the same (-1.7%).
